# Optimization experiments

Measured on AMD Instinct MI355X. Metric: run time of the kernel, lower is better.

## Reference

```python
import jax, jax.numpy as jnp
import numpy as np

VOCAB, EMBED, HID, MAXLEN, BATCH = 32000, 512, 512, 64, 32
DEC_H = 2 * HID  # decoder hidden width = 2*hidden_size


def _lstm_cell(x, h, c, wx, wh, b):
    # PyTorch LSTMCell gate order: i, f, g, o
    gates = x @ wx + h @ wh + b
    i, f, g, o = jnp.split(gates, 4, axis=-1)
    c = jax.nn.sigmoid(f) * c + jax.nn.sigmoid(i) * jnp.tanh(g)
    h = jax.nn.sigmoid(o) * jnp.tanh(c)
    return h, c


def setup_inputs() -> dict:
    key = jax.random.key(0)
    ks = jax.random.split(key, 12)
    s = 0.02
    inp = {
        "x": jax.random.randint(ks[0], (BATCH, MAXLEN), 0, VOCAB),
        # encoder: embedding [V, E], LSTM cell E -> 2H
        "enc_embed": jax.random.normal(ks[1], (VOCAB, EMBED), jnp.float32) * s,
        "enc_wx": jax.random.normal(ks[2], (EMBED, 4 * DEC_H), jnp.float32) * s,
        "enc_wh": jax.random.normal(ks[3], (DEC_H, 4 * DEC_H), jnp.float32) * s,
        "enc_b": jnp.zeros((4 * DEC_H,), jnp.float32),
        # decoder: embedding [V, 2H], Bahdanau attn, combine, LSTM cell 2H -> 2H, out proj
        "dec_embed": jax.random.normal(ks[4], (VOCAB, DEC_H), jnp.float32) * s,
        "attn_w": jax.random.normal(ks[5], (2 * DEC_H, MAXLEN), jnp.float32) * s,
        "attn_b": jnp.zeros((MAXLEN,), jnp.float32),
        "comb_w": jax.random.normal(ks[6], (2 * DEC_H, DEC_H), jnp.float32) * s,
        "comb_b": jnp.zeros((DEC_H,), jnp.float32),
        "dec_wx": jax.random.normal(ks[7], (DEC_H, 4 * DEC_H), jnp.float32) * s,
        "dec_wh": jax.random.normal(ks[8], (DEC_H, 4 * DEC_H), jnp.float32) * s,
        "dec_b": jnp.zeros((4 * DEC_H,), jnp.float32),
        "out_w": jax.random.normal(ks[9], (DEC_H, VOCAB), jnp.float32) * s,
        "out_b": jnp.zeros((VOCAB,), jnp.float32),
    }
    return inp


def reference(x, enc_embed, enc_wx, enc_wh, enc_b, dec_embed, attn_w, attn_b,
              comb_w, comb_b, dec_wx, dec_wh, dec_b, out_w, out_b):
    B = x.shape[0]

    # ---- encoder: one token per step, scan over time ----
    def enc_step(carry, tok):
        h, c = carry
        e = enc_embed[tok]  # (B, E)
        h, c = _lstm_cell(e, h, c, enc_wx, enc_wh, enc_b)
        return (h, c), h

    h0 = jnp.zeros((B, DEC_H), jnp.float32)
    (_, _), enc_outs = jax.lax.scan(enc_step, (h0, h0), x.T)  # (L, B, 2H)
    enc_outs = enc_outs.transpose(1, 0, 2)  # (B, L, 2H)

    # ---- decoder: Bahdanau attention + greedy feedback, scan over steps ----
    def dec_step(carry, _):
        h, c, tok = carry
        e = dec_embed[tok]  # (B, 2H)
        aw = jax.nn.softmax(jnp.concatenate([e, h], -1) @ attn_w + attn_b, -1)  # (B, L)
        ctx = jnp.einsum('bl,bld->bd', aw, enc_outs)  # (B, 2H)
        inp = jax.nn.relu(jnp.concatenate([e, ctx], -1) @ comb_w + comb_b)
        h, c = _lstm_cell(inp, h, c, dec_wx, dec_wh, dec_b)
        logp = jax.nn.log_softmax(h @ out_w + out_b, -1)  # (B, V)
        tok = jnp.argmax(logp, -1)
        return (h, c, tok), logp

    tok0 = jnp.full((B,), 127, dtype=x.dtype)
    (_, _, _), outs = jax.lax.scan(dec_step, (h0, h0, tok0), None, length=MAXLEN)
    return outs.transpose(1, 0, 2)  # (B, L, V)
```

## Files before the change

### kernel.cpp

```cpp
#include <hip/hip_runtime.h>

#define B   32
#define L   64
#define DH  1024
#define G4  4096
#define EK  512
#define V   32000

__device__ __forceinline__ float sigm(float x){ return 1.f/(1.f+expf(-x)); }
__device__ __forceinline__ unsigned mono(float f){
  unsigned u = __float_as_uint(f);
  return (u & 0x80000000u) ? ~u : (u | 0x80000000u);
}

__global__ __launch_bounds__(256) void init_kernel(float* h, float* c){
  int i = blockIdx.x*256 + threadIdx.x;
  if (i < B*DH){ h[i]=0.f; c[i]=0.f; }
}

__global__ __launch_bounds__(256) void gates_kernel(
    int mode, int t,
    const int* __restrict__ x, const float* __restrict__ embed,
    const float* __restrict__ src1, int K1,
    const float* __restrict__ wx, const float* __restrict__ wh,
    const float* __restrict__ bias,
    const float* __restrict__ h_in, float* __restrict__ h_out,
    float* __restrict__ cst, float* __restrict__ enc_outs)
{
  __shared__ float es[128][36];
  __shared__ int tok_s[B];
  __shared__ float gate_s[4][8][B];
  int tid = threadIdx.x;
  int hc = tid & 7, g = (tid>>3)&3, rg = tid>>5;
  int jh = blockIdx.x*8 + hc;
  int jg = g*DH + jh;
  float a0=0.f,a1=0.f,a2=0.f,a3=0.f;
  if (mode==0 && tid < B) tok_s[tid] = x[tid*L + t];
  __syncthreads();
  for (int phase=0; phase<2; ++phase){
    int K = phase ? DH : K1;
    const float* W = phase ? wh : wx;
    for (int kb=0; kb<K; kb+=128){
      for (int i=0;i<16;++i){
        int idx = i*256 + tid;
        int b = idx >> 7, kk = idx & 127;
        int k = kb + kk;
        float v;
        if (phase)          v = h_in[b*DH + k];
        else if (mode==0)   v = embed[(long)tok_s[b]*EK + k];
        else { v = src1[b*DH + k]; v = v>0.f ? v : 0.f; }
        es[kk][b] = v;
      }
      __syncthreads();
      #pragma unroll 8
      for (int kk=0; kk<128; ++kk){
        float w = W[(long)(kb+kk)*G4 + jg];
        float4 hv = *reinterpret_cast<const float4*>(&es[kk][rg*4]);
        a0 += hv.x*w; a1 += hv.y*w; a2 += hv.z*w; a3 += hv.w*w;
      }
      __syncthreads();
    }
  }
  float bj = bias[jg];
  gate_s[g][hc][rg*4+0] = a0+bj;
  gate_s[g][hc][rg*4+1] = a1+bj;
  gate_s[g][hc][rg*4+2] = a2+bj;
  gate_s[g][hc][rg*4+3] = a3+bj;
  __syncthreads();
  if (tid < 64){
    int hc2 = tid & 7, rg2 = tid >> 3;
    int j = blockIdx.x*8 + hc2;
    for (int i=0;i<4;++i){
      int b = rg2*4 + i;
      float iv = gate_s[0][hc2][b];
      float fv = gate_s[1][hc2][b];
      float gv = gate_s[2][hc2][b];
      float ov = gate_s[3][hc2][b];
      float cn = sigm(fv)*cst[b*DH + j] + sigm(iv)*tanhf(gv);
      cst[b*DH + j] = cn;
      float hv = sigm(ov)*tanhf(cn);
      h_out[b*DH + j] = hv;
      if (enc_outs) enc_outs[((long)b*L + t)*DH + j] = hv;
    }
  }
}

__global__ __launch_bounds__(256) void attn_kernel(
    int t, const unsigned long long* __restrict__ ptok,
    const float* __restrict__ dec_embed, const float* __restrict__ attn_w,
    const float* __restrict__ attn_b, const float* __restrict__ h_in,
    const float* __restrict__ enc_outs,
    float* __restrict__ e_buf, float* __restrict__ ctx,
    float* __restrict__ inp, const float* __restrict__ comb_b)
{
  __shared__ float e_s[DH], h_s[DH], sc_s[4][64], aw_s[64];
  __shared__ int tok_sh;
  int b = blockIdx.x, tid = threadIdx.x;
  if (tid==0){
    int tok = 127;
    if (t > 0) tok = (int)(~(unsigned)(ptok[(t-1)*B + b] & 0xffffffffull));
    tok_sh = tok;
  }
  __syncthreads();
  int tok = tok_sh;
  for (int i=0;i<4;++i){
    int k = i*256 + tid;
    float ev = dec_embed[(long)tok*DH + k];
    float hv = h_in[b*DH + k];
    e_s[k]=ev; h_s[k]=hv;
    e_buf[b*DH + k] = ev;
    inp[b*DH + k] = comb_b[k];
  }
  __syncthreads();
  int l = tid & 63, ks = tid >> 6;
  float p = 0.f;
  for (int kk=0; kk<512; ++kk){
    int k = ks*512 + kk;
    float sv = (k < DH) ? e_s[k] : h_s[k-DH];
    p += sv * attn_w[(long)k*64 + l];
  }
  sc_s[ks][l] = p;
  __syncthreads();
  if (tid < 64){
    float s = sc_s[0][l]+sc_s[1][l]+sc_s[2][l]+sc_s[3][l] + attn_b[l];
    float m = s;
    for (int off=32; off; off>>=1) m = fmaxf(m, __shfl_xor(m, off));
    float e = expf(s-m);
    float sum = e;
    for (int off=32; off; off>>=1) sum += __shfl_xor(sum, off);
    aw_s[l] = e/sum;
  }
  __syncthreads();
  float c0=0.f,c1=0.f,c2=0.f,c3=0.f;
  for (int ll=0; ll<64; ++ll){
    float a = aw_s[ll];
    const float* er = &enc_outs[((long)b*L + ll)*DH];
    c0 += a*er[tid]; c1 += a*er[256+tid]; c2 += a*er[512+tid]; c3 += a*er[768+tid];
  }
  ctx[b*DH + tid]       = c0;
  ctx[b*DH + 256 + tid] = c1;
  ctx[b*DH + 512 + tid] = c2;
  ctx[b*DH + 768 + tid] = c3;
}

__global__ __launch_bounds__(256) void comb_kernel(
    const float* __restrict__ e_buf, const float* __restrict__ ctx,
    const float* __restrict__ comb_w, float* __restrict__ inp)
{
  __shared__ float es[128][36];
  int tid = threadIdx.x;
  int col = tid & 31, rg = tid >> 5;
  int j = blockIdx.x*32 + col;
  int kr = blockIdx.y;
  const float* src = (kr < 2) ? e_buf : ctx;
  int kbase0 = (kr & 1)*512;
  float a0=0.f,a1=0.f,a2=0.f,a3=0.f;
  for (int kb=0; kb<512; kb+=128){
    for (int i=0;i<16;++i){
      int idx = i*256 + tid;
      int b = idx >> 7, kk = idx & 127;
      es[kk][b] = src[b*DH + kbase0 + kb + kk];
    }
    __syncthreads();
    #pragma unroll 8
    for (int kk=0; kk<128; ++kk){
      float w = comb_w[(long)(kr*512 + kb + kk)*DH + j];
      float4 hv = *reinterpret_cast<const float4*>(&es[kk][rg*4]);
      a0 += hv.x*w; a1 += hv.y*w; a2 += hv.z*w; a3 += hv.w*w;
    }
    __syncthreads();
  }
  atomicAdd(&inp[(rg*4+0)*DH + j], a0);
  atomicAdd(&inp[(rg*4+1)*DH + j], a1);
  atomicAdd(&inp[(rg*4+2)*DH + j], a2);
  atomicAdd(&inp[(rg*4+3)*DH + j], a3);
}

__global__ __launch_bounds__(256) void outproj_kernel(
    int t, const float* __restrict__ hsrc, const float* __restrict__ out_w,
    const float* __restrict__ out_b, float* __restrict__ out,
    float* __restrict__ psum, unsigned long long* __restrict__ pmax)
{
  __shared__ float hs[128][36];
  __shared__ float red_s[B][33];
  __shared__ unsigned long long pk_s[B][33];
  int tid = threadIdx.x;
  int col = tid & 31, rg = tid >> 5;
  int j = blockIdx.x*32 + col;
  float a0=0.f,a1=0.f,a2=0.f,a3=0.f;
  for (int kb=0; kb<DH; kb+=128){
    for (int i=0;i<16;++i){
      int idx = i*256 + tid;
      int b = idx >> 7, kk = idx & 127;
      hs[kk][b] = hsrc[b*DH + kb + kk];
    }
    __syncthreads();
    #pragma unroll 8
    for (int kk=0; kk<128; ++kk){
      float w = out_w[(long)(kb+kk)*V + j];
      float4 hv = *reinterpret_cast<const float4*>(&hs[kk][rg*4]);
      a0 += hv.x*w; a1 += hv.y*w; a2 += hv.z*w; a3 += hv.w*w;
    }
    __syncthreads();
  }
  float bj = out_b[j];
  float lg0=a0+bj, lg1=a1+bj, lg2=a2+bj, lg3=a3+bj;
  int r0 = rg*4;
  out[((long)(r0+0)*L + t)*V + j] = lg0;
  out[((long)(r0+1)*L + t)*V + j] = lg1;
  out[((long)(r0+2)*L + t)*V + j] = lg2;
  out[((long)(r0+3)*L + t)*V + j] = lg3;
  unsigned nj = ~(unsigned)j;
  red_s[r0+0][col] = expf(lg0);
  red_s[r0+1][col] = expf(lg1);
  red_s[r0+2][col] = expf(lg2);
  red_s[r0+3][col] = expf(lg3);
  pk_s[r0+0][col] = ((unsigned long long)mono(lg0)<<32) | nj;
  pk_s[r0+1][col] = ((unsigned long long)mono(lg1)<<32) | nj;
  pk_s[r0+2][col] = ((unsigned long long)mono(lg2)<<32) | nj;
  pk_s[r0+3][col] = ((unsigned long long)mono(lg3)<<32) | nj;
  __syncthreads();
  if (tid < B){
    float s = 0.f; unsigned long long mx = 0ull;
    for (int cc=0; cc<32; ++cc){
      s += red_s[tid][cc];
      unsigned long long v = pk_s[tid][cc];
      if (v > mx) mx = v;
    }
    psum[tid*1024 + blockIdx.x] = s;
    pmax[tid*1024 + blockIdx.x] = mx;
  }
}

__global__ __launch_bounds__(256) void reduce_kernel(
    int t, const float* __restrict__ psum, const unsigned long long* __restrict__ pmax,
    float* __restrict__ lse, unsigned long long* __restrict__ ptok)
{
  __shared__ float ss[256];
  __shared__ unsigned long long ms[256];
  int row = blockIdx.x, tid = threadIdx.x;
  float s = 0.f; unsigned long long mx = 0ull;
  for (int i=tid; i<1000; i+=256){
    s += psum[row*1024 + i];
    unsigned long long v = pmax[row*1024 + i];
    if (v > mx) mx = v;
  }
  ss[tid]=s; ms[tid]=mx;
  __syncthreads();
  for (int off=128; off; off>>=1){
    if (tid < off){
      ss[tid] += ss[tid+off];
      if (ms[tid+off] > ms[tid]) ms[tid] = ms[tid+off];
    }
    __syncthreads();
  }
  if (tid==0){
    lse[t*B + row] = logf(ss[0]);
    ptok[t*B + row] = ms[0];
  }
}

__global__ __launch_bounds__(256) void norm_kernel(
    int t, float* __restrict__ out, const float* __restrict__ lse)
{
  int v = blockIdx.x*256 + threadIdx.x;
  int b = blockIdx.y;
  out[((long)b*L + t)*V + v] -= lse[t*B + b];
}

extern "C" void kernel_launch(void* const* d_in, const int* in_sizes, int n_in,
                              void* d_out, int out_size, void* d_ws, size_t ws_size,
                              hipStream_t stream)
{
  const int*   x         = (const int*)  d_in[0];
  const float* enc_embed = (const float*)d_in[1];
  const float* enc_wx    = (const float*)d_in[2];
  const float* enc_wh    = (const float*)d_in[3];
  const float* enc_b     = (const float*)d_in[4];
  const float* dec_embed = (const float*)d_in[5];
  const float* attn_w    = (const float*)d_in[6];
  const float* attn_b    = (const float*)d_in[7];
  const float* comb_w    = (const float*)d_in[8];
  const float* comb_b    = (const float*)d_in[9];
  const float* dec_wx    = (const float*)d_in[10];
  const float* dec_wh    = (const float*)d_in[11];
  const float* dec_b     = (const float*)d_in[12];
  const float* out_w     = (const float*)d_in[13];
  const float* out_b     = (const float*)d_in[14];
  float* out = (float*)d_out;

  float* enc_outs = (float*)d_ws;
  float* h0    = enc_outs + (size_t)B*L*DH;
  float* h1    = h0 + B*DH;
  float* c     = h1 + B*DH;
  float* e_buf = c  + B*DH;
  float* ctx   = e_buf + B*DH;
  float* inp   = ctx + B*DH;
  float* psum  = inp + B*DH;
  float* lse   = psum + B*1024;
  unsigned long long* pmax = (unsigned long long*)(lse + L*B);
  unsigned long long* ptok = pmax + B*1024;

  init_kernel<<<128,256,0,stream>>>(h0, c);
  for (int t=0; t<L; ++t){
    const float* hi = (t&1) ? h1 : h0;
    float*       ho = (t&1) ? h0 : h1;
    gates_kernel<<<128,256,0,stream>>>(0, t, x, enc_embed, nullptr, EK,
        enc_wx, enc_wh, enc_b, hi, ho, c, enc_outs);
  }
  init_kernel<<<128,256,0,stream>>>(h0, c);
  for (int t=0; t<L; ++t){
    const float* hi = (t&1) ? h1 : h0;
    float*       ho = (t&1) ? h0 : h1;
    attn_kernel<<<B,256,0,stream>>>(t, ptok, dec_embed, attn_w, attn_b,
        hi, enc_outs, e_buf, ctx, inp, comb_b);
    comb_kernel<<<dim3(32,4),256,0,stream>>>(e_buf, ctx, comb_w, inp);
    gates_kernel<<<128,256,0,stream>>>(1, t, nullptr, nullptr, inp, DH,
        dec_wx, dec_wh, dec_b, hi, ho, c, nullptr);
    outproj_kernel<<<1000,256,0,stream>>>(t, ho, out_w, out_b, out, psum, pmax);
    reduce_kernel<<<B,256,0,stream>>>(t, psum, pmax, lse, ptok);
    norm_kernel<<<dim3(125,B),256,0,stream>>>(t, out, lse);
  }
}
```

Before: 28.80 ms.

## Split-K gate GEMVs, float4 register tiling, fuse argmax reduce into attention

The LSTM gate matmul becomes a split-K kernel that writes partial gates, followed by a separate cell kernel that sums the partials and applies the nonlinearity. The gates, combine and output-projection kernels now use float4 weight loads with a 4x4 register tile per thread to cut load instructions and raise reuse. The per-step log-sum-exp/argmax reduction moves into the next step's attention kernel, and the per-step normalization is batched into one launch after the loop, removing two launches per decoder step. The costs are extra global traffic for the gate partials and one additional cell launch per step.

```diff
diff --git a/kernel.cpp b/kernel.cpp
--- a/kernel.cpp
+++ b/kernel.cpp
@@ -6,6 +6,8 @@
 #define G4  4096
 #define EK  512
 #define V   32000
+#define NPB 250
+#define ESTR 264
 
 __device__ __forceinline__ float sigm(float x){ return 1.f/(1.f+expf(-x)); }
 __device__ __forceinline__ unsigned mono(float f){
@@ -23,157 +25,221 @@
     const int* __restrict__ x, const float* __restrict__ embed,
     const float* __restrict__ src1, int K1,
     const float* __restrict__ wx, const float* __restrict__ wh,
-    const float* __restrict__ bias,
-    const float* __restrict__ h_in, float* __restrict__ h_out,
-    float* __restrict__ cst, float* __restrict__ enc_outs)
-{
-  __shared__ float es[128][36];
+    const float* __restrict__ h_in, float* __restrict__ gp)
+{
+  __shared__ float es[B][ESTR];
   __shared__ int tok_s[B];
-  __shared__ float gate_s[4][8][B];
   int tid = threadIdx.x;
-  int hc = tid & 7, g = (tid>>3)&3, rg = tid>>5;
-  int jh = blockIdx.x*8 + hc;
-  int jg = g*DH + jh;
-  float a0=0.f,a1=0.f,a2=0.f,a3=0.f;
-  if (mode==0 && tid < B) tok_s[tid] = x[tid*L + t];
-  __syncthreads();
-  for (int phase=0; phase<2; ++phase){
-    int K = phase ? DH : K1;
-    const float* W = phase ? wh : wx;
-    for (int kb=0; kb<K; kb+=128){
-      for (int i=0;i<16;++i){
-        int idx = i*256 + tid;
-        int b = idx >> 7, kk = idx & 127;
-        int k = kb + kk;
-        float v;
-        if (phase)          v = h_in[b*DH + k];
-        else if (mode==0)   v = embed[(long)tok_s[b]*EK + k];
-        else { v = src1[b*DH + k]; v = v>0.f ? v : 0.f; }
-        es[kk][b] = v;
+  int cb = blockIdx.x, ch = blockIdx.y;
+  int ks0 = ch*256;
+  const float* W; int krow0;
+  if (ks0 < K1){ W = wx; krow0 = ks0; } else { W = wh; krow0 = ks0 - K1; }
+  if (mode==0 && ks0 < K1 && tid < B) tok_s[tid] = x[tid*L + t];
+  __syncthreads();
+  {
+    int bb = tid >> 3;
+    int m  = (tid & 7) * 4;
+    const float* srow;
+    bool do_relu = false;
+    if (ks0 < K1){
+      if (mode==0) srow = embed + (size_t)tok_s[bb]*EK + ks0;
+      else { srow = src1 + (size_t)bb*DH + ks0; do_relu = true; }
+    } else {
+      srow = h_in + (size_t)bb*DH + (ks0 - K1);
+    }
+    #pragma unroll
+    for (int p=0; p<8; ++p){
+      int k = p*32 + m;
+      float4 v = *reinterpret_cast<const float4*>(srow + k);
+      if (do_relu){
+        v.x = fmaxf(v.x,0.f); v.y = fmaxf(v.y,0.f);
+        v.z = fmaxf(v.z,0.f); v.w = fmaxf(v.w,0.f);
       }
-      __syncthreads();
-      #pragma unroll 8
-      for (int kk=0; kk<128; ++kk){
-        float w = W[(long)(kb+kk)*G4 + jg];
-        float4 hv = *reinterpret_cast<const float4*>(&es[kk][rg*4]);
-        a0 += hv.x*w; a1 += hv.y*w; a2 += hv.z*w; a3 += hv.w*w;
-      }
-      __syncthreads();
-    }
-  }
-  float bj = bias[jg];
-  gate_s[g][hc][rg*4+0] = a0+bj;
-  gate_s[g][hc][rg*4+1] = a1+bj;
-  gate_s[g][hc][rg*4+2] = a2+bj;
-  gate_s[g][hc][rg*4+3] = a3+bj;
-  __syncthreads();
-  if (tid < 64){
-    int hc2 = tid & 7, rg2 = tid >> 3;
-    int j = blockIdx.x*8 + hc2;
-    for (int i=0;i<4;++i){
-      int b = rg2*4 + i;
-      float iv = gate_s[0][hc2][b];
-      float fv = gate_s[1][hc2][b];
-      float gv = gate_s[2][hc2][b];
-      float ov = gate_s[3][hc2][b];
-      float cn = sigm(fv)*cst[b*DH + j] + sigm(iv)*tanhf(gv);
-      cst[b*DH + j] = cn;
-      float hv = sigm(ov)*tanhf(cn);
-      h_out[b*DH + j] = hv;
-      if (enc_outs) enc_outs[((long)b*L + t)*DH + j] = hv;
-    }
-  }
+      *reinterpret_cast<float4*>(&es[bb][k]) = v;
+    }
+  }
+  __syncthreads();
+  int cg = tid & 31, rg = tid >> 5;
+  int j  = cb*128 + cg*4;
+  int r0 = rg*4;
+  float4 a0={0,0,0,0}, a1={0,0,0,0}, a2={0,0,0,0}, a3={0,0,0,0};
+  const float* wp = W + (size_t)krow0*G4 + j;
+  #pragma unroll 16
+  for (int k=0; k<256; ++k){
+    float4 w = *reinterpret_cast<const float4*>(wp + (size_t)k*G4);
+    float x0 = es[r0+0][k], x1 = es[r0+1][k], x2 = es[r0+2][k], x3 = es[r0+3][k];
+    a0.x += x0*w.x; a0.y += x0*w.y; a0.z += x0*w.z; a0.w += x0*w.w;
+    a1.x += x1*w.x; a1.y += x1*w.y; a1.z += x1*w.z; a1.w += x1*w.w;
+    a2.x += x2*w.x; a2.y += x2*w.y; a2.z += x2*w.z; a2.w += x2*w.w;
+    a3.x += x3*w.x; a3.y += x3*w.y; a3.z += x3*w.z; a3.w += x3*w.w;
+  }
+  float* gpr = gp + ((size_t)ch*B)*G4 + j;
+  *reinterpret_cast<float4*>(gpr + (size_t)(r0+0)*G4) = a0;
+  *reinterpret_cast<float4*>(gpr + (size_t)(r0+1)*G4) = a1;
+  *reinterpret_cast<float4*>(gpr + (size_t)(r0+2)*G4) = a2;
+  *reinterpret_cast<float4*>(gpr + (size_t)(r0+3)*G4) = a3;
+}
+
+__global__ __launch_bounds__(256) void cell_kernel(
+    int CH, int t, const float* __restrict__ gp, const float* __restrict__ bias,
+    float* __restrict__ cst, float* __restrict__ h_out, float* __restrict__ enc_outs)
+{
+  int idx = blockIdx.x*256 + threadIdx.x;
+  int b = idx >> 10, jj = idx & 1023;
+  float gi = bias[jj], gf = bias[DH+jj], gg = bias[2*DH+jj], go = bias[3*DH+jj];
+  const float* g0 = gp + (size_t)b*G4 + jj;
+  if (CH == 8){
+    #pragma unroll
+    for (int ch=0; ch<8; ++ch){
+      const float* g = g0 + (size_t)ch*B*G4;
+      gi += g[0]; gf += g[DH]; gg += g[2*DH]; go += g[3*DH];
+    }
+  } else {
+    #pragma unroll
+    for (int ch=0; ch<6; ++ch){
+      const float* g = g0 + (size_t)ch*B*G4;
+      gi += g[0]; gf += g[DH]; gg += g[2*DH]; go += g[3*DH];
+    }
+  }
+  float cn = sigm(gf)*cst[idx] + sigm(gi)*tanhf(gg);
+  cst[idx] = cn;
+  float hv = sigm(go)*tanhf(cn);
+  h_out[idx] = hv;
+  if (enc_outs) enc_outs[((size_t)b*L + t)*DH + jj] = hv;
 }
 
 __global__ __launch_bounds__(256) void attn_kernel(
-    int t, const unsigned long long* __restrict__ ptok,
+    int t, const float* __restrict__ psum, const unsigned long long* __restrict__ pmax,
+    float* __restrict__ lse,
     const float* __restrict__ dec_embed, const float* __restrict__ attn_w,
     const float* __restrict__ attn_b, const float* __restrict__ h_in,
     const float* __restrict__ enc_outs,
-    float* __restrict__ e_buf, float* __restrict__ ctx,
+    float* __restrict__ e_buf, float* __restrict__ ctxv,
     float* __restrict__ inp, const float* __restrict__ comb_b)
 {
-  __shared__ float e_s[DH], h_s[DH], sc_s[4][64], aw_s[64];
+  __shared__ float cat_s[2*DH];
+  __shared__ float sc_s[16][68];
+  __shared__ float aw_s[64];
+  __shared__ float rs[256];
+  __shared__ unsigned long long rm[256];
   __shared__ int tok_sh;
   int b = blockIdx.x, tid = threadIdx.x;
-  if (tid==0){
-    int tok = 127;
-    if (t > 0) tok = (int)(~(unsigned)(ptok[(t-1)*B + b] & 0xffffffffull));
-    tok_sh = tok;
+  if (t > 0){
+    float s = 0.f; unsigned long long mx = 0ull;
+    for (int i=tid; i<NPB; i+=256){
+      s += psum[b*256 + i];
+      unsigned long long v = pmax[b*256 + i];
+      if (v > mx) mx = v;
+    }
+    rs[tid] = s; rm[tid] = mx;
+    __syncthreads();
+    for (int off=128; off; off>>=1){
+      if (tid < off){
+        rs[tid] += rs[tid+off];
+        if (rm[tid+off] > rm[tid]) rm[tid] = rm[tid+off];
+      }
+      __syncthreads();
+    }
+    if (tid==0){
+      lse[(t-1)*B + b] = logf(rs[0]);
+      tok_sh = (int)(~(unsigned)(rm[0] & 0xffffffffull));
+    }
+  } else {
+    if (tid==0) tok_sh = 127;
   }
   __syncthreads();
   int tok = tok_sh;
+  #pragma unroll
   for (int i=0;i<4;++i){
     int k = i*256 + tid;
-    float ev = dec_embed[(long)tok*DH + k];
+    float ev = dec_embed[(size_t)tok*DH + k];
     float hv = h_in[b*DH + k];
-    e_s[k]=ev; h_s[k]=hv;
+    cat_s[k] = ev; cat_s[DH + k] = hv;
     e_buf[b*DH + k] = ev;
     inp[b*DH + k] = comb_b[k];
   }
   __syncthreads();
-  int l = tid & 63, ks = tid >> 6;
-  float p = 0.f;
-  for (int kk=0; kk<512; ++kk){
-    int k = ks*512 + kk;
-    float sv = (k < DH) ? e_s[k] : h_s[k-DH];
-    p += sv * attn_w[(long)k*64 + l];
-  }
-  sc_s[ks][l] = p;
+  {
+    int lg = tid & 15, ks = tid >> 4;
+    float4 p = {0,0,0,0};
+    const float* wp = attn_w + (size_t)(ks*128)*64 + lg*4;
+    #pragma unroll 8
+    for (int kk=0; kk<128; ++kk){
+      float4 w = *reinterpret_cast<const float4*>(wp + (size_t)kk*64);
+      float xv = cat_s[ks*128 + kk];
+      p.x += xv*w.x; p.y += xv*w.y; p.z += xv*w.z; p.w += xv*w.w;
+    }
+    *reinterpret_cast<float4*>(&sc_s[ks][lg*4]) = p;
+  }
   __syncthreads();
   if (tid < 64){
-    float s = sc_s[0][l]+sc_s[1][l]+sc_s[2][l]+sc_s[3][l] + attn_b[l];
+    float s = attn_b[tid];
+    #pragma unroll
+    for (int ks=0; ks<16; ++ks) s += sc_s[ks][tid];
     float m = s;
     for (int off=32; off; off>>=1) m = fmaxf(m, __shfl_xor(m, off));
-    float e = expf(s-m);
+    float e = expf(s - m);
     float sum = e;
     for (int off=32; off; off>>=1) sum += __shfl_xor(sum, off);
-    aw_s[l] = e/sum;
+    aw_s[tid] = e/sum;
   }
   __syncthreads();
   float c0=0.f,c1=0.f,c2=0.f,c3=0.f;
+  const float* eb = enc_outs + (size_t)b*L*DH;
+  #pragma unroll 8
   for (int ll=0; ll<64; ++ll){
     float a = aw_s[ll];
-    const float* er = &enc_outs[((long)b*L + ll)*DH];
+    const float* er = eb + (size_t)ll*DH;
     c0 += a*er[tid]; c1 += a*er[256+tid]; c2 += a*er[512+tid]; c3 += a*er[768+tid];
   }
-  ctx[b*DH + tid]       = c0;
-  ctx[b*DH + 256 + tid] = c1;
-  ctx[b*DH + 512 + tid] = c2;
-  ctx[b*DH + 768 + tid] = c3;
+  ctxv[b*DH + tid]       = c0;
+  ctxv[b*DH + 256 + tid] = c1;
+  ctxv[b*DH + 512 + tid] = c2;
+  ctxv[b*DH + 768 + tid] = c3;
 }
 
 __global__ __launch_bounds__(256) void comb_kernel(
-    const float* __restrict__ e_buf, const float* __restrict__ ctx,
+    const float* __restrict__ e_buf, const float* __restrict__ ctxv,
     const float* __restrict__ comb_w, float* __restrict__ inp)
 {
-  __shared__ float es[128][36];
+  __shared__ float es[B][ESTR];
   int tid = threadIdx.x;
-  int col = tid & 31, rg = tid >> 5;
-  int j = blockIdx.x*32 + col;
-  int kr = blockIdx.y;
-  const float* src = (kr < 2) ? e_buf : ctx;
-  int kbase0 = (kr & 1)*512;
-  float a0=0.f,a1=0.f,a2=0.f,a3=0.f;
-  for (int kb=0; kb<512; kb+=128){
-    for (int i=0;i<16;++i){
-      int idx = i*256 + tid;
-      int b = idx >> 7, kk = idx & 127;
-      es[kk][b] = src[b*DH + kbase0 + kb + kk];
-    }
-    __syncthreads();
-    #pragma unroll 8
-    for (int kk=0; kk<128; ++kk){
-      float w = comb_w[(long)(kr*512 + kb + kk)*DH + j];
-      float4 hv = *reinterpret_cast<const float4*>(&es[kk][rg*4]);
-      a0 += hv.x*w; a1 += hv.y*w; a2 += hv.z*w; a3 += hv.w*w;
-    }
-    __syncthreads();
-  }
-  atomicAdd(&inp[(rg*4+0)*DH + j], a0);
-  atomicAdd(&inp[(rg*4+1)*DH + j], a1);
-  atomicAdd(&inp[(rg*4+2)*DH + j], a2);
-  atomicAdd(&inp[(rg*4+3)*DH + j], a3);
+  int cb = blockIdx.x, ch = blockIdx.y;
+  int ks0 = ch*256;
+  const float* src; int off;
+  if (ks0 < DH){ src = e_buf; off = ks0; } else { src = ctxv; off = ks0 - DH; }
+  {
+    int bb = tid >> 3, m = (tid & 7)*4;
+    const float* srow = src + (size_t)bb*DH + off;
+    #pragma unroll
+    for (int p=0; p<8; ++p){
+      int k = p*32 + m;
+      *reinterpret_cast<float4*>(&es[bb][k]) = *reinterpret_cast<const float4*>(srow + k);
+    }
+  }
+  __syncthreads();
+  int cg = tid & 31, rg = tid >> 5;
+  int j  = cb*128 + cg*4;
+  int r0 = rg*4;
+  float4 a0={0,0,0,0}, a1={0,0,0,0}, a2={0,0,0,0}, a3={0,0,0,0};
+  const float* wp = comb_w + (size_t)ks0*DH + j;
+  #pragma unroll 16
+  for (int k=0; k<256; ++k){
+    float4 w = *reinterpret_cast<const float4*>(wp + (size_t)k*DH);
+    float x0 = es[r0+0][k], x1 = es[r0+1][k], x2 = es[r0+2][k], x3 = es[r0+3][k];
+    a0.x += x0*w.x; a0.y += x0*w.y; a0.z += x0*w.z; a0.w += x0*w.w;
+    a1.x += x1*w.x; a1.y += x1*w.y; a1.z += x1*w.z; a1.w += x1*w.w;
+    a2.x += x2*w.x; a2.y += x2*w.y; a2.z += x2*w.z; a2.w += x2*w.w;
+    a3.x += x3*w.x; a3.y += x3*w.y; a3.z += x3*w.z; a3.w += x3*w.w;
+  }
+  float* p0 = inp + (size_t)(r0+0)*DH + j;
+  float* p1 = inp + (size_t)(r0+1)*DH + j;
+  float* p2 = inp + (size_t)(r0+2)*DH + j;
+  float* p3 = inp + (size_t)(r0+3)*DH + j;
+  atomicAdd(p0+0,a0.x); atomicAdd(p0+1,a0.y); atomicAdd(p0+2,a0.z); atomicAdd(p0+3,a0.w);
+  atomicAdd(p1+0,a1.x); atomicAdd(p1+1,a1.y); atomicAdd(p1+2,a1.z); atomicAdd(p1+3,a1.w);
+  atomicAdd(p2+0,a2.x); atomicAdd(p2+1,a2.y); atomicAdd(p2+2,a2.z); atomicAdd(p2+3,a2.w);
+  atomicAdd(p3+0,a3.x); atomicAdd(p3+1,a3.y); atomicAdd(p3+2,a3.z); atomicAdd(p3+3,a3.w);
 }
 
 __global__ __launch_bounds__(256) void outproj_kernel(
@@ -181,91 +247,95 @@
     const float* __restrict__ out_b, float* __restrict__ out,
     float* __restrict__ psum, unsigned long long* __restrict__ pmax)
 {
-  __shared__ float hs[128][36];
+  __shared__ float hs[256][36];
   __shared__ float red_s[B][33];
   __shared__ unsigned long long pk_s[B][33];
   int tid = threadIdx.x;
-  int col = tid & 31, rg = tid >> 5;
-  int j = blockIdx.x*32 + col;
-  float a0=0.f,a1=0.f,a2=0.f,a3=0.f;
-  for (int kb=0; kb<DH; kb+=128){
-    for (int i=0;i<16;++i){
-      int idx = i*256 + tid;
-      int b = idx >> 7, kk = idx & 127;
-      hs[kk][b] = hsrc[b*DH + kb + kk];
+  int cg = tid & 31, rg = tid >> 5;
+  int j  = blockIdx.x*128 + cg*4;
+  int r0 = rg*4;
+  float4 a0={0,0,0,0}, a1={0,0,0,0}, a2={0,0,0,0}, a3={0,0,0,0};
+  for (int kb=0; kb<DH; kb+=256){
+    {
+      int bb = tid >> 3, m = (tid & 7)*4;
+      const float* hrow = hsrc + (size_t)bb*DH + kb;
+      #pragma unroll
+      for (int p=0; p<8; ++p){
+        int k = p*32 + m;
+        float4 v = *reinterpret_cast<const float4*>(hrow + k);
+        hs[k+0][bb]=v.x; hs[k+1][bb]=v.y; hs[k+2][bb]=v.z; hs[k+3][bb]=v.w;
+      }
     }
     __syncthreads();
-    #pragma unroll 8
-    for (int kk=0; kk<128; ++kk){
-      float w = out_w[(long)(kb+kk)*V + j];
-      float4 hv = *reinterpret_cast<const float4*>(&hs[kk][rg*4]);
-      a0 += hv.x*w; a1 += hv.y*w; a2 += hv.z*w; a3 += hv.w*w;
+    const float* wp = out_w + (size_t)kb*V + j;
+    #pragma unroll 16
+    for (int k=0; k<256; ++k){
+      float4 w  = *reinterpret_cast<const float4*>(wp + (size_t)k*V);
+      float4 hv = *reinterpret_cast<const float4*>(&hs[k][r0]);
+      a0.x += hv.x*w.x; a0.y += hv.x*w.y; a0.z += hv.x*w.z; a0.w += hv.x*w.w;
+      a1.x += hv.y*w.x; a1.y += hv.y*w.y; a1.z += hv.y*w.z; a1.w += hv.y*w.w;
+      a2.x += hv.z*w.x; a2.y += hv.z*w.y; a2.z += hv.z*w.z; a2.w += hv.z*w.w;
+      a3.x += hv.w*w.x; a3.y += hv.w*w.y; a3.z += hv.w*w.z; a3.w += hv.w*w.w;
     }
     __syncthreads();
   }
-  float bj = out_b[j];
-  float lg0=a0+bj, lg1=a1+bj, lg2=a2+bj, lg3=a3+bj;
-  int r0 = rg*4;
-  out[((long)(r0+0)*L + t)*V + j] = lg0;
-  out[((long)(r0+1)*L + t)*V + j] = lg1;
-  out[((long)(r0+2)*L + t)*V + j] = lg2;
-  out[((long)(r0+3)*L + t)*V + j] = lg3;
-  unsigned nj = ~(unsigned)j;
-  red_s[r0+0][col] = expf(lg0);
-  red_s[r0+1][col] = expf(lg1);
-  red_s[r0+2][col] = expf(lg2);
-  red_s[r0+3][col] = expf(lg3);
-  pk_s[r0+0][col] = ((unsigned long long)mono(lg0)<<32) | nj;
-  pk_s[r0+1][col] = ((unsigned long long)mono(lg1)<<32) | nj;
-  pk_s[r0+2][col] = ((unsigned long long)mono(lg2)<<32) | nj;
-  pk_s[r0+3][col] = ((unsigned long long)mono(lg3)<<32) | nj;
+  float4 bb4 = *reinterpret_cast<const float4*>(out_b + j);
+  float4 lg[4];
+  lg[0].x = a0.x+bb4.x; lg[0].y = a0.y+bb4.y; lg[0].z = a0.z+bb4.z; lg[0].w = a0.w+bb4.w;
+  lg[1].x = a1.x+bb4.x; lg[1].y = a1.y+bb4.y; lg[1].z = a1.z+bb4.z; lg[1].w = a1.w+bb4.w;
+  lg[2].x = a2.x+bb4.x; lg[2].y = a2.y+bb4.y; lg[2].z = a2.z+bb4.z; lg[2].w = a2.w+bb4.w;
+  lg[3].x = a3.x+bb4.x; lg[3].y = a3.y+bb4.y; lg[3].z = a3.z+bb4.z; lg[3].w = a3.w+bb4.w;
+  #pragma unroll
+  for (int r=0; r<4; ++r){
+    int b = r0 + r;
+    *reinterpret_cast<float4*>(&out[((size_t)b*L + t)*V + j]) = lg[r];
+    float se = expf(lg[r].x) + expf(lg[r].y) + expf(lg[r].z) + expf(lg[r].w);
+    unsigned long long m0 = ((unsigned long long)mono(lg[r].x)<<32) | (~(unsigned)(j+0));
+    unsigned long long m1 = ((unsigned long long)mono(lg[r].y)<<32) | (~(unsigned)(j+1));
+    unsigned long long m2 = ((unsigned long long)mono(lg[r].z)<<32) | (~(unsigned)(j+2));
+    unsigned long long m3 = ((unsigned long long)mono(lg[r].w)<<32) | (~(unsigned)(j+3));
+    if (m1 > m0) m0 = m1;
+    if (m3 > m2) m2 = m3;
+    if (m2 > m0) m0 = m2;
+    red_s[b][cg] = se;
+    pk_s[b][cg]  = m0;
+  }
   __syncthreads();
   if (tid < B){
     float s = 0.f; unsigned long long mx = 0ull;
+    #pragma unroll 8
     for (int cc=0; cc<32; ++cc){
       s += red_s[tid][cc];
       unsigned long long v = pk_s[tid][cc];
       if (v > mx) mx = v;
     }
-    psum[tid*1024 + blockIdx.x] = s;
-    pmax[tid*1024 + blockIdx.x] = mx;
-  }
-}
-
-__global__ __launch_bounds__(256) void reduce_kernel(
-    int t, const float* __restrict__ psum, const unsigned long long* __restrict__ pmax,
-    float* __restrict__ lse, unsigned long long* __restrict__ ptok)
-{
-  __shared__ float ss[256];
-  __shared__ unsigned long long ms[256];
-  int row = blockIdx.x, tid = threadIdx.x;
-  float s = 0.f; unsigned long long mx = 0ull;
-  for (int i=tid; i<1000; i+=256){
-    s += psum[row*1024 + i];
-    unsigned long long v = pmax[row*1024 + i];
-    if (v > mx) mx = v;
-  }
-  ss[tid]=s; ms[tid]=mx;
+    psum[tid*256 + blockIdx.x] = s;
+    pmax[tid*256 + blockIdx.x] = mx;
+  }
+}
+
+__global__ __launch_bounds__(256) void lastlse_kernel(
+    const float* __restrict__ psum, float* __restrict__ lse)
+{
+  __shared__ float rs[256];
+  int b = blockIdx.x, tid = threadIdx.x;
+  float s = 0.f;
+  for (int i=tid; i<NPB; i+=256) s += psum[b*256 + i];
+  rs[tid] = s;
   __syncthreads();
   for (int off=128; off; off>>=1){
-    if (tid < off){
-      ss[tid] += ss[tid+off];
-      if (ms[tid+off] > ms[tid]) ms[tid] = ms[tid+off];
-    }
+    if (tid < off) rs[tid] += rs[tid+off];
     __syncthreads();
   }
-  if (tid==0){
-    lse[t*B + row] = logf(ss[0]);
-    ptok[t*B + row] = ms[0];
-  }
+  if (tid==0) lse[(L-1)*B + b] = logf(rs[0]);
 }
 
 __global__ __launch_bounds__(256) void norm_kernel(
-    int t, float* __restrict__ out, const float* __restrict__ lse)
+    float* __restrict__ out, const float* __restrict__ lse)
 {
   int v = blockIdx.x*256 + threadIdx.x;
-  int b = blockIdx.y;
-  out[((long)b*L + t)*V + v] -= lse[t*B + b];
+  int b = blockIdx.y, t = blockIdx.z;
+  out[((size_t)b*L + t)*V + v] -= lse[t*B + b];
 }
 
 extern "C" void kernel_launch(void* const* d_in, const int* in_sizes, int n_in,
@@ -294,31 +364,33 @@
   float* h1    = h0 + B*DH;
   float* c     = h1 + B*DH;
   float* e_buf = c  + B*DH;
-  float* ctx   = e_buf + B*DH;
-  float* inp   = ctx + B*DH;
-  float* psum  = inp + B*DH;
-  float* lse   = psum + B*1024;
+  float* ctxv  = e_buf + B*DH;
+  float* inp   = ctxv + B*DH;
+  float* gpart = inp + B*DH;
+  float* psum  = gpart + (size_t)8*B*G4;
+  float* lse   = psum + B*256;
   unsigned long long* pmax = (unsigned long long*)(lse + L*B);
-  unsigned long long* ptok = pmax + B*1024;
 
   init_kernel<<<128,256,0,stream>>>(h0, c);
   for (int t=0; t<L; ++t){
     const float* hi = (t&1) ? h1 : h0;
     float*       ho = (t&1) ? h0 : h1;
-    gates_kernel<<<128,256,0,stream>>>(0, t, x, enc_embed, nullptr, EK,
-        enc_wx, enc_wh, enc_b, hi, ho, c, enc_outs);
+    gates_kernel<<<dim3(32,6),256,0,stream>>>(0, t, x, enc_embed, nullptr, EK,
+        enc_wx, enc_wh, hi, gpart);
+    cell_kernel<<<128,256,0,stream>>>(6, t, gpart, enc_b, c, ho, enc_outs);
   }
   init_kernel<<<128,256,0,stream>>>(h0, c);
   for (int t=0; t<L; ++t){
     const float* hi = (t&1) ? h1 : h0;
     float*       ho = (t&1) ? h0 : h1;
-    attn_kernel<<<B,256,0,stream>>>(t, ptok, dec_embed, attn_w, attn_b,
-        hi, enc_outs, e_buf, ctx, inp, comb_b);
-    comb_kernel<<<dim3(32,4),256,0,stream>>>(e_buf, ctx, comb_w, inp);
-    gates_kernel<<<128,256,0,stream>>>(1, t, nullptr, nullptr, inp, DH,
-        dec_wx, dec_wh, dec_b, hi, ho, c, nullptr);
-    outproj_kernel<<<1000,256,0,stream>>>(t, ho, out_w, out_b, out, psum, pmax);
-    reduce_kernel<<<B,256,0,stream>>>(t, psum, pmax, lse, ptok);
-    norm_kernel<<<dim3(125,B),256,0,stream>>>(t, out, lse);
-  }
-}
+    attn_kernel<<<B,256,0,stream>>>(t, psum, pmax, lse, dec_embed, attn_w, attn_b,
+        hi, enc_outs, e_buf, ctxv, inp, comb_b);
+    comb_kernel<<<dim3(8,8),256,0,stream>>>(e_buf, ctxv, comb_w, inp);
+    gates_kernel<<<dim3(32,8),256,0,stream>>>(1, t, nullptr, nullptr, inp, DH,
+        dec_wx, dec_wh, hi, gpart);
+    cell_kernel<<<128,256,0,stream>>>(8, t, gpart, dec_b, c, ho, nullptr);
+    outproj_kernel<<<NPB,256,0,stream>>>(t, ho, out_w, out_b, out, psum, pmax);
+  }
+  lastlse_kernel<<<B,256,0,stream>>>(psum, lse);
+  norm_kernel<<<dim3(125,B,L),256,0,stream>>>(out, lse);
+}
```

Result: slower. 31.88 ms (+10.7%).
